# Optimization experiments

Measured on AMD Instinct MI355X. Metric: run time of the kernel, lower is better.

Reference implementation:

```python
import jax, jax.numpy as jnp
import numpy as np

DIM = 16
N_HEADS = 4
HEAD_DIM = DIM // N_HEADS
B = 2097152


def setup_inputs() -> dict:
    key = jax.random.key(0)
    k1, k2, k3, k4, k5, k6 = jax.random.split(key, 6)
    return {
        "fp_16": jax.random.normal(k1, (B, DIM), dtype=jnp.float32),
        "chem_16": jax.random.normal(k2, (B, DIM), dtype=jnp.float32),
        "in_proj_weight": jax.random.normal(k3, (3 * DIM, DIM), dtype=jnp.float32) * 0.25,
        "in_proj_bias": jax.random.normal(k4, (3 * DIM,), dtype=jnp.float32) * 0.02,
        "out_proj_weight": jax.random.normal(k5, (DIM, DIM), dtype=jnp.float32) * 0.25,
        "out_proj_bias": jax.random.normal(k6, (DIM,), dtype=jnp.float32) * 0.02,
    }


def reference(fp_16, chem_16, in_proj_weight, in_proj_bias, out_proj_weight, out_proj_bias):
    # nn.MultiheadAttention packed QKV projection split
    Wq, Wk, Wv = in_proj_weight[:DIM], in_proj_weight[DIM:2 * DIM], in_proj_weight[2 * DIM:]
    bq, bk, bv = in_proj_bias[:DIM], in_proj_bias[DIM:2 * DIM], in_proj_bias[2 * DIM:]

    q = fp_16 @ Wq.T + bq      # (B, 16)
    k = chem_16 @ Wk.T + bk    # (B, 16)
    v = chem_16 @ Wv.T + bv    # (B, 16)

    # Single-token attention: seq_len_q = seq_len_kv = 1.
    # Per-head scores (B, H, 1, 1); softmax over a length-1 key axis is exactly 1,
    # so attn_out == v. Computed explicitly for faithfulness (cheap at this scale).
    qh = q.reshape(B, N_HEADS, HEAD_DIM)
    kh = k.reshape(B, N_HEADS, HEAD_DIM)
    vh = v.reshape(B, N_HEADS, HEAD_DIM)
    scores = jnp.einsum("bhd,bhd->bh", qh, kh) / jnp.sqrt(jnp.float32(HEAD_DIM))
    w = jax.nn.softmax(scores[..., None], axis=-1)  # (B, H, 1) -> all ones
    attn = (w * vh.reshape(B, N_HEADS, 1, HEAD_DIM).squeeze(2)[..., None, :].squeeze(-2)[..., None] * 0 + vh) if False else w[..., 0:1] * vh  # (B, H, hd)
    attn = attn.reshape(B, DIM)

    return attn @ out_proj_weight.T + out_proj_bias  # (B, 16)
```

## Files before the change

### kernel.cpp

```cpp
#include <hip/hip_runtime.h>


#define DIM 16
#define BATCH 2097152

__global__ void fold_weights_kernel(const float* __restrict__ in_proj_weight,
                                    const float* __restrict__ in_proj_bias,
                                    const float* __restrict__ out_proj_weight,
                                    const float* __restrict__ out_proj_bias,
                                    float* __restrict__ ws) {
    int t = threadIdx.x;
    int j = t >> 4;
    int i = t & 15;
    float acc = 0.0f;
#pragma unroll
    for (int k = 0; k < 16; ++k)
        acc += out_proj_weight[j * 16 + k] * in_proj_weight[(32 + k) * 16 + i];
    ws[t] = acc;
    if (t < 16) {
        float b = out_proj_bias[t];
#pragma unroll
        for (int k = 0; k < 16; ++k)
            b += out_proj_weight[t * 16 + k] * in_proj_bias[32 + k];
        ws[256 + t] = b;
    }
}

__device__ __forceinline__ float4 shfl_xor_f4(float4 v, int mask) {
    float4 r;
    r.x = __shfl_xor(v.x, mask, 64);
    r.y = __shfl_xor(v.y, mask, 64);
    r.z = __shfl_xor(v.z, mask, 64);
    r.w = __shfl_xor(v.w, mask, 64);
    return r;
}

__global__ __launch_bounds__(256) void affine_rows_coalesced(
    const float* __restrict__ x,
    const float* __restrict__ wfold,
    float* __restrict__ out) {
    const int t = threadIdx.x;
    const int q = t & 3;

    float4 w[4][4];
#pragma unroll
    for (int m = 0; m < 4; ++m) {
        const int qc = q ^ m;
#pragma unroll
        for (int jp = 0; jp < 4; ++jp)
            w[m][jp] = *(const float4*)(wfold + (q * 4 + jp) * 16 + qc * 4);
    }
    const float4 bias = *(const float4*)(wfold + 256 + q * 4);

    const float4* xv = (const float4*)x;
    float4* ov = (float4*)out;
    const size_t base = (size_t)blockIdx.x * 1024;

#pragma unroll
    for (int k = 0; k < 4; ++k) {
        const size_t idx = base + (size_t)k * 256 + t;
        float4 xs0 = xv[idx];
        float4 xs1 = shfl_xor_f4(xs0, 1);
        float4 xs2 = shfl_xor_f4(xs0, 2);
        float4 xs3 = shfl_xor_f4(xs0, 3);

        float4 acc = bias;
#define ACCUM(m, xsv)                                                   \
        acc.x += xsv.x * w[m][0].x + xsv.y * w[m][0].y +                \
                 xsv.z * w[m][0].z + xsv.w * w[m][0].w;                 \
        acc.y += xsv.x * w[m][1].x + xsv.y * w[m][1].y +                \
                 xsv.z * w[m][1].z + xsv.w * w[m][1].w;                 \
        acc.z += xsv.x * w[m][2].x + xsv.y * w[m][2].y +                \
                 xsv.z * w[m][2].z + xsv.w * w[m][2].w;                 \
        acc.w += xsv.x * w[m][3].x + xsv.y * w[m][3].y +                \
                 xsv.z * w[m][3].z + xsv.w * w[m][3].w;
        ACCUM(0, xs0)
        ACCUM(1, xs1)
        ACCUM(2, xs2)
        ACCUM(3, xs3)
#undef ACCUM

        ov[idx] = acc;
    }
}

extern "C" void kernel_launch(void* const* d_in, const int* in_sizes, int n_in,
                              void* d_out, int out_size, void* d_ws, size_t ws_size,
                              hipStream_t stream) {
    const float* chem        = (const float*)d_in[1];
    const float* in_proj_w   = (const float*)d_in[2];
    const float* in_proj_b   = (const float*)d_in[3];
    const float* out_proj_w  = (const float*)d_in[4];
    const float* out_proj_b  = (const float*)d_in[5];
    float* out = (float*)d_out;
    float* ws  = (float*)d_ws;

    fold_weights_kernel<<<1, 256, 0, stream>>>(in_proj_w, in_proj_b,
                                               out_proj_w, out_proj_b, ws);

    const int blocks = BATCH / 256;
    affine_rows_coalesced<<<blocks, 256, 0, stream>>>(chem, ws, out);
}
```

Measured before the change: 285.9 us.

## Fuse weight folding into affine kernel and use nontemporal loads/stores

Removes the separate single-block weight-folding launch. Every block now recomputes the folded 16x16 weight and bias into shared memory before its rows are processed. Input loads and output stores switch to nontemporal builtins to avoid polluting the cache on this streaming pass. The trade-off is redundant per-block folding work (about 16 FMAs per thread plus small global reads) and a __syncthreads in exchange for dropping one kernel launch and its dependency.

```diff
diff --git a/kernel.cpp b/kernel.cpp
--- a/kernel.cpp
+++ b/kernel.cpp
@@ -4,30 +4,10 @@
 #define DIM 16
 #define BATCH 2097152
 
-__global__ void fold_weights_kernel(const float* __restrict__ in_proj_weight,
-                                    const float* __restrict__ in_proj_bias,
-                                    const float* __restrict__ out_proj_weight,
-                                    const float* __restrict__ out_proj_bias,
-                                    float* __restrict__ ws) {
-    int t = threadIdx.x;
-    int j = t >> 4;
-    int i = t & 15;
-    float acc = 0.0f;
-#pragma unroll
-    for (int k = 0; k < 16; ++k)
-        acc += out_proj_weight[j * 16 + k] * in_proj_weight[(32 + k) * 16 + i];
-    ws[t] = acc;
-    if (t < 16) {
-        float b = out_proj_bias[t];
-#pragma unroll
-        for (int k = 0; k < 16; ++k)
-            b += out_proj_weight[t * 16 + k] * in_proj_bias[32 + k];
-        ws[256 + t] = b;
-    }
-}
+typedef float f4 __attribute__((ext_vector_type(4)));
 
-__device__ __forceinline__ float4 shfl_xor_f4(float4 v, int mask) {
-    float4 r;
+__device__ __forceinline__ f4 shfl_xor_f4(f4 v, int mask) {
+    f4 r;
     r.x = __shfl_xor(v.x, mask, 64);
     r.y = __shfl_xor(v.y, mask, 64);
     r.z = __shfl_xor(v.z, mask, 64);
@@ -35,36 +15,59 @@
     return r;
 }
 
-__global__ __launch_bounds__(256) void affine_rows_coalesced(
+__global__ __launch_bounds__(256) void fused_affine(
     const float* __restrict__ x,
-    const float* __restrict__ wfold,
+    const float* __restrict__ in_proj_weight,
+    const float* __restrict__ in_proj_bias,
+    const float* __restrict__ out_proj_weight,
+    const float* __restrict__ out_proj_bias,
     float* __restrict__ out) {
+    __shared__ __align__(16) float wfold[272];
+
     const int t = threadIdx.x;
+
+    {
+        const int j = t >> 4;
+        const int i = t & 15;
+        float acc = 0.0f;
+#pragma unroll
+        for (int k = 0; k < 16; ++k)
+            acc += out_proj_weight[j * 16 + k] * in_proj_weight[(32 + k) * 16 + i];
+        wfold[t] = acc;
+        if (t < 16) {
+            float b = out_proj_bias[t];
+#pragma unroll
+            for (int k = 0; k < 16; ++k)
+                b += out_proj_weight[t * 16 + k] * in_proj_bias[32 + k];
+            wfold[256 + t] = b;
+        }
+    }
+    __syncthreads();
+
     const int q = t & 3;
-
-    float4 w[4][4];
+    f4 w[4][4];
 #pragma unroll
     for (int m = 0; m < 4; ++m) {
         const int qc = q ^ m;
 #pragma unroll
         for (int jp = 0; jp < 4; ++jp)
-            w[m][jp] = *(const float4*)(wfold + (q * 4 + jp) * 16 + qc * 4);
+            w[m][jp] = *(const f4*)(wfold + (q * 4 + jp) * 16 + qc * 4);
     }
-    const float4 bias = *(const float4*)(wfold + 256 + q * 4);
+    const f4 bias = *(const f4*)(wfold + 256 + q * 4);
 
-    const float4* xv = (const float4*)x;
-    float4* ov = (float4*)out;
+    const f4* xv = (const f4*)x;
+    f4* ov = (f4*)out;
     const size_t base = (size_t)blockIdx.x * 1024;
 
 #pragma unroll
     for (int k = 0; k < 4; ++k) {
         const size_t idx = base + (size_t)k * 256 + t;
-        float4 xs0 = xv[idx];
-        float4 xs1 = shfl_xor_f4(xs0, 1);
-        float4 xs2 = shfl_xor_f4(xs0, 2);
-        float4 xs3 = shfl_xor_f4(xs0, 3);
+        f4 xs0 = __builtin_nontemporal_load(xv + idx);
+        f4 xs1 = shfl_xor_f4(xs0, 1);
+        f4 xs2 = shfl_xor_f4(xs0, 2);
+        f4 xs3 = shfl_xor_f4(xs0, 3);
 
-        float4 acc = bias;
+        f4 acc = bias;
 #define ACCUM(m, xsv)                                                   \
         acc.x += xsv.x * w[m][0].x + xsv.y * w[m][0].y +                \
                  xsv.z * w[m][0].z + xsv.w * w[m][0].w;                 \
@@ -80,7 +83,7 @@
         ACCUM(3, xs3)
 #undef ACCUM
 
-        ov[idx] = acc;
+        __builtin_nontemporal_store(acc, ov + idx);
     }
 }
 
@@ -93,11 +96,8 @@
     const float* out_proj_w  = (const float*)d_in[4];
     const float* out_proj_b  = (const float*)d_in[5];
     float* out = (float*)d_out;
-    float* ws  = (float*)d_ws;
-
-    fold_weights_kernel<<<1, 256, 0, stream>>>(in_proj_w, in_proj_b,
-                                               out_proj_w, out_proj_b, ws);
 
     const int blocks = BATCH / 256;
-    affine_rows_coalesced<<<blocks, 256, 0, stream>>>(chem, ws, out);
+    fused_affine<<<blocks, 256, 0, stream>>>(chem, in_proj_w, in_proj_b,
+                                             out_proj_w, out_proj_b, out);
 }
```

Measured after the change: 282.4 us. About the same (-1.2%).
